# Kernel optimization log

Hardware: AMD Instinct MI355X
Metric: run time of the kernel (lower is better)

Reference implementation:

```python
import jax, jax.numpy as jnp
import numpy as np

B, S, D = 4, 2048, 1024


def setup_inputs() -> dict:
    key = jax.random.key(0)
    ks = jax.random.split(key, 9)
    scale = 1.0 / np.sqrt(D)
    x = jax.random.normal(ks[0], (B, S, D), dtype=jnp.float32)
    mask = jnp.tril(jnp.ones((S, S), dtype=jnp.int32))[None, :, :]  # causal, broadcast over batch
    Wq = jax.random.normal(ks[1], (D, D), dtype=jnp.float32) * scale
    bq = jax.random.normal(ks[2], (D,), dtype=jnp.float32) * 0.01
    Wk = jax.random.normal(ks[3], (D, D), dtype=jnp.float32) * scale
    bk = jax.random.normal(ks[4], (D,), dtype=jnp.float32) * 0.01
    Wv = jax.random.normal(ks[5], (D, D), dtype=jnp.float32) * scale
    bv = jax.random.normal(ks[6], (D,), dtype=jnp.float32) * 0.01
    Wo = jax.random.normal(ks[7], (D, D), dtype=jnp.float32) * scale
    bo = jax.random.normal(ks[8], (D,), dtype=jnp.float32) * 0.01
    return {"x": x, "mask": mask, "Wq": Wq, "bq": bq, "Wk": Wk, "bk": bk,
            "Wv": Wv, "bv": bv, "Wo": Wo, "bo": bo}


def reference(x, mask, Wq, bq, Wk, bk, Wv, bv, Wo, bo):
    # Linear projections (torch Linear: x @ W^T + b; here W stored as [in, out])
    Q = jnp.einsum('bsd,de->bse', x, Wq) + bq
    K = jnp.einsum('bsd,de->bse', x, Wk) + bk
    V = jnp.einsum('bsd,de->bse', x, Wv) + bv
    d_k = Q.shape[-1]
    scores = jnp.einsum('bqd,bkd->bqk', Q, K) / jnp.sqrt(jnp.float32(d_k))
    scores = jnp.where(mask == 0, jnp.float32(-jnp.inf), scores)
    attn_weights = jax.nn.softmax(scores, axis=-1)  # [B, S, S]
    attn_output = jnp.einsum('bqk,bkd->bqd', attn_weights, V)
    output = jnp.einsum('bsd,de->bse', attn_output, Wo) + bo
    return output, attn_weights
```

## Files before the change

kernel.cpp:

```cpp
#include <hip/hip_runtime.h>
#include <cstdint>
#include <cstddef>
#include <cmath>

typedef __bf16 bf16_t;
typedef bf16_t bf16x8 __attribute__((ext_vector_type(8)));
typedef bf16_t bf16x4 __attribute__((ext_vector_type(4)));
typedef float f32x4 __attribute__((ext_vector_type(4)));

constexpr int kB = 4;
constexpr int kS = 2048;
constexpr int kD = 1024;
constexpr int BM = 128, BN = 128, BK = 32;
constexpr int TILE_ELEMS = (BM + BN) * BK;

typedef __attribute__((address_space(1))) void as1void;
typedef __attribute__((address_space(3))) void as3void;

__device__ __forceinline__ void gload16(const void* g, void* l) {
  __builtin_amdgcn_global_load_lds((as1void*)g, (as3void*)l, 16, 0, 0);
}

__device__ __forceinline__ void wgbar() {
  asm volatile("" ::: "memory");
  __builtin_amdgcn_s_barrier();
  asm volatile("" ::: "memory");
}

__device__ __forceinline__ void gemm_mainloop(
    const bf16_t* __restrict__ A, int lda,
    const bf16_t* __restrict__ B, int ldb,
    int ksteps, bf16_t* lds, f32x4 acc[4][4]) {
  const int tid = threadIdx.x;
  const int w = tid >> 6, lane = tid & 63;
  const int srow = lane >> 2;
  const int scol = (lane & 3) << 3;
  const int wr = (w >> 1) << 6, wc = (w & 1) << 6;
  const int fr = lane & 15, kg = lane >> 4;

  const bf16_t* ga0 = A + (size_t)(w * 16 + srow) * lda + scol;
  const bf16_t* ga1 = A + (size_t)(64 + w * 16 + srow) * lda + scol;
  const bf16_t* gb0 = B + (size_t)(w * 16 + srow) * ldb + scol;
  const bf16_t* gb1 = B + (size_t)(64 + w * 16 + srow) * ldb + scol;
  const int oa0 = (w * 16) * BK;
  const int oa1 = (64 + w * 16) * BK;
  const int ob0 = BM * BK + (w * 16) * BK;
  const int ob1 = BM * BK + (64 + w * 16) * BK;

  gload16(ga0, lds + oa0);
  gload16(ga1, lds + oa1);
  gload16(gb0, lds + ob0);
  gload16(gb1, lds + ob1);
  ga0 += BK; ga1 += BK; gb0 += BK; gb1 += BK;
  __syncthreads();

  int cur = 0;
  for (int ks = 0; ks < ksteps; ++ks) {
    const int nxt = cur ^ 1;
    if (ks + 1 < ksteps) {
      bf16_t* nb = lds + nxt * TILE_ELEMS;
      gload16(ga0, nb + oa0);
      gload16(ga1, nb + oa1);
      gload16(gb0, nb + ob0);
      gload16(gb1, nb + ob1);
      ga0 += BK; ga1 += BK; gb0 += BK; gb1 += BK;
    }
    const bf16_t* cb = lds + cur * TILE_ELEMS;
    bf16x8 af[4], bfv[4];
#pragma unroll
    for (int m = 0; m < 4; ++m)
      af[m] = *(const bf16x8*)(cb + (wr + m * 16 + fr) * BK + kg * 8);
#pragma unroll
    for (int n = 0; n < 4; ++n)
      bfv[n] = *(const bf16x8*)(cb + BM * BK + (wc + n * 16 + fr) * BK + kg * 8);
#pragma unroll
    for (int m = 0; m < 4; ++m)
#pragma unroll
      for (int n = 0; n < 4; ++n)
        acc[m][n] = __builtin_amdgcn_mfma_f32_16x16x32_bf16(af[m], bfv[n],
                                                            acc[m][n], 0, 0, 0);
    __syncthreads();
    cur = nxt;
  }
}

__device__ __forceinline__ void gemm256_loop(
    const bf16_t* __restrict__ A, int lda,
    const bf16_t* __restrict__ B, int ldb,
    int nk, bf16_t* lds, f32x4 acc[8][4]) {
  const int tid = threadIdx.x;
  const int wid = tid >> 6, lane = tid & 63;
  const int wm = wid >> 2, wn = wid & 3;
  const int fr = lane & 15, kg = (lane >> 4) & 3;
  const int s_row = ((tid >> 7) << 4) | (tid & 15);
  const int s_col = ((tid >> 4) & 7) << 3;
  const bf16_t* pA = A + (size_t)s_row * lda + s_col;
  const bf16_t* pB = B + (size_t)s_row * ldb + s_col;
  const int ldst = wid << 9;

  auto stg = [&](int tt, int op, int h, int j) {
    const bf16_t* g = (op ? pB : pA) + (size_t)(h * 128 + j * 64) * (op ? ldb : lda)
                      + (size_t)tt * 64;
    bf16_t* d = lds + (((tt & 1) * 4 + op * 2 + h) * 8192) + j * 4096 + ldst;
    gload16(g, d);
  };

#pragma unroll
  for (int h = 0; h < 2; ++h)
#pragma unroll
    for (int j = 0; j < 2; ++j) { stg(0, 0, h, j); stg(0, 1, h, j); }
  stg(1, 1, 0, 0); stg(1, 1, 0, 1); stg(1, 1, 1, 0); stg(1, 1, 1, 1);
  stg(1, 0, 0, 0); stg(1, 0, 1, 0);
  asm volatile("s_waitcnt vmcnt(6)" ::: "memory");
  wgbar();

  const int arow = kg * 128 + fr * 8;
  for (int t = 0; t < nk; ++t) {
    const bf16_t* sb = lds + (t & 1) * 32768;
    const bf16_t* aslot = sb + wm * 8192;
    const bf16_t* bslot = sb + (2 + (wn >> 1)) * 8192 + (wn & 1) * 4096;
    bf16x8 bF[4][2];
#pragma unroll
    for (int q = 0; q < 4; ++q) {
      bf16x8 aF[2][2];
#pragma unroll
      for (int mi = 0; mi < 2; ++mi)
#pragma unroll
        for (int ks = 0; ks < 2; ++ks)
          aF[mi][ks] = *(const bf16x8*)(aslot + (2 * q + mi) * 1024 + ks * 512 + arow);
      if (q == 0) {
#pragma unroll
        for (int n = 0; n < 4; ++n)
#pragma unroll
          for (int ks = 0; ks < 2; ++ks)
            bF[n][ks] = *(const bf16x8*)(bslot + n * 1024 + ks * 512 + arow);
      }
      if (q == 0)      { if (t + 1 <= nk - 1) { stg(t + 1, 0, 0, 1); stg(t + 1, 0, 1, 1); } }
      else if (q == 1) { if (t + 2 <= nk - 1) { stg(t + 2, 1, 0, 0); stg(t + 2, 1, 0, 1); } }
      else if (q == 2) { if (t + 2 <= nk - 1) { stg(t + 2, 1, 1, 0); stg(t + 2, 1, 1, 1); } }
      else             { if (t + 2 <= nk - 1) { stg(t + 2, 0, 0, 0); stg(t + 2, 0, 1, 0); } }
      wgbar();
      __builtin_amdgcn_s_setprio(1);
#pragma unroll
      for (int mi = 0; mi < 2; ++mi)
#pragma unroll
        for (int n = 0; n < 4; ++n)
#pragma unroll
          for (int ks = 0; ks < 2; ++ks)
            acc[2 * q + mi][n] = __builtin_amdgcn_mfma_f32_16x16x32_bf16(
                aF[mi][ks], bF[n][ks], acc[2 * q + mi][n], 0, 0, 0);
      __builtin_amdgcn_s_setprio(0);
      asm volatile("s_waitcnt lgkmcnt(0)" ::: "memory");
      if (q == 3 && t < nk - 1) {
        if (t + 2 <= nk - 1) asm volatile("s_waitcnt vmcnt(6)" ::: "memory");
        else                 asm volatile("s_waitcnt vmcnt(0)" ::: "memory");
      }
      wgbar();
    }
  }
}


__global__ __launch_bounds__(512, 2)
void k_qk256(const bf16_t* __restrict__ A, const bf16_t* __restrict__ WT,
             const float* __restrict__ bq, const float* __restrict__ bk,
             bf16_t* __restrict__ Qb, bf16_t* __restrict__ Kb) {
  __shared__ bf16_t lds[65536];
  const int id = blockIdx.x;
  const int swz = (id & 7) * 32 + (id >> 3);
  const int mb = swz >> 3, nb = swz & 7;
  const int m0 = mb * 256, n0 = nb * 256;
  f32x4 acc[8][4] = {};
  gemm256_loop(A + (size_t)m0 * kD, kD, WT + (size_t)n0 * kD, kD,
               kD / 64, lds, acc);
  const int lane = threadIdx.x & 63, wid = threadIdx.x >> 6;
  const int wm = wid >> 2, wn = wid & 3, fr = lane & 15, kgr = lane >> 4;
  const int which = n0 >> 10;
  bf16_t* C = which == 0 ? Qb : Kb;
  const float* bias = which == 0 ? bq : bk;
#pragma unroll
  for (int n = 0; n < 4; ++n) {
    const int col = (n0 & 1023) + wn * 64 + n * 16 + fr;
    const float bvv = bias[col];
#pragma unroll
    for (int m = 0; m < 8; ++m)
#pragma unroll
      for (int i = 0; i < 4; ++i) {
        const int row = m0 + wm * 128 + m * 16 + kgr * 4 + i;
        C[(size_t)row * kD + col] = (bf16_t)(acc[m][n][i] + bvv);
      }
  }
}

__global__ __launch_bounds__(256)
void k_scores_v(const bf16_t* __restrict__ Q, const bf16_t* __restrict__ K,
                float* __restrict__ Sc,
                const bf16_t* __restrict__ X, const bf16_t* __restrict__ WvT,
                const float* __restrict__ bv, bf16_t* __restrict__ VT) {
  __shared__ bf16_t lds[2 * TILE_ELEMS];
  const int id = blockIdx.x;
  const int wid0 = (id & 7) * 192 + (id >> 3);
  const int tid = threadIdx.x, w = tid >> 6, lane = tid & 63;
  const int wr = (w >> 1) << 6, wc = (w & 1) << 6, fr = lane & 15, kg = lane >> 4;
  if (wid0 < 544) {
    const int b = wid0 / 136, t = wid0 % 136;
    int by = (int)((sqrtf(8.f * t + 1.f) - 1.f) * 0.5f);
    while ((by + 1) * (by + 2) / 2 <= t) ++by;
    while (by * (by + 1) / 2 > t) --by;
    const int bx = t - by * (by + 1) / 2;
    const int m0 = by * BM, n0 = bx * BN;
    f32x4 acc[4][4] = {};
    gemm_mainloop(Q + (size_t)b * kS * kD + (size_t)m0 * kD, kD,
                  K + (size_t)b * kS * kD + (size_t)n0 * kD, kD, kD / BK, lds, acc);
    float* Sb = Sc + (size_t)b * kS * kS;
#pragma unroll
    for (int m = 0; m < 4; ++m)
#pragma unroll
      for (int n = 0; n < 4; ++n)
#pragma unroll
        for (int i = 0; i < 4; ++i) {
          const int row = m0 + wr + m * 16 + kg * 4 + i;
          const int col = n0 + wc + n * 16 + fr;
          Sb[(size_t)row * kS + col] = acc[m][n][i] * 0.03125f;
        }
  } else if (wid0 < 1024) {
    const int zid = wid0 - 544;
    const int b = zid / 120, u = zid % 120;
    int r = (int)((1.f + sqrtf(8.f * u + 1.f)) * 0.5f);
    while (r * (r - 1) / 2 > u) --r;
    while ((r + 1) * r / 2 <= u) ++r;
    const int c = u - r * (r - 1) / 2;
    const int by = c, bx = r;
    float* base = Sc + (size_t)b * kS * kS + (size_t)by * BM * kS + bx * BN;
    const f32x4 z = {0.f, 0.f, 0.f, 0.f};
    for (int i = tid; i < 128 * 32; i += 256) {
      const int row = i >> 5, c4 = i & 31;
      ((f32x4*)(base + (size_t)row * kS))[c4] = z;
    }
  } else {
    const int vid = wid0 - 1024;
    const int m0 = (vid >> 3) * BM, n0 = (vid & 7) * BN;
    f32x4 acc[4][4] = {};
    gemm_mainloop(X + (size_t)m0 * kD, kD, WvT + (size_t)n0 * kD, kD,
                  kD / BK, lds, acc);
#pragma unroll
    for (int n = 0; n < 4; ++n) {
      const int col = n0 + wc + n * 16 + fr;
      const float bvv = bv[col];
#pragma unroll
      for (int m = 0; m < 4; ++m)
#pragma unroll
        for (int i = 0; i < 4; ++i) {
          const int row = m0 + wr + m * 16 + kg * 4 + i;
          const int b = row >> 11, s = row & (kS - 1);
          VT[((size_t)b * kD + col) * kS + s] = (bf16_t)(acc[m][n][i] + bvv);
        }
    }
  }
}

__global__ __launch_bounds__(256)
void k_softmax(float* __restrict__ P, bf16_t* __restrict__ Pb) {
  const int row = blockIdx.x;
  const int q = row & (kS - 1);
  const int L = q + 1;
  const int nch = (q >> 2) + 1;
  const int nB = ((q & ~127) + 128) >> 2;
  float* p = P + (size_t)row * kS;
  f32x4* p4 = (f32x4*)p;
  bf16x4* pb4 = (bf16x4*)(Pb + (size_t)row * kS);
  const int tid = threadIdx.x;
  const int c0 = tid, c1 = 256 + tid;
  f32x4 v0 = {-1e30f, -1e30f, -1e30f, -1e30f}, v1 = v0;
  if (c0 < nch) v0 = p4[c0];
  if (c1 < nch) v1 = p4[c1];
#pragma unroll
  for (int j = 0; j < 4; ++j) {
    if (4 * c0 + j >= L) v0[j] = -1e30f;
    if (4 * c1 + j >= L) v1[j] = -1e30f;
  }
  float mx = -1e30f;
#pragma unroll
  for (int j = 0; j < 4; ++j) mx = fmaxf(mx, fmaxf(v0[j], v1[j]));
#pragma unroll
  for (int s2 = 32; s2 >= 1; s2 >>= 1) mx = fmaxf(mx, __shfl_xor(mx, s2));
  __shared__ float red[8];
  if ((tid & 63) == 0) red[tid >> 6] = mx;
  __syncthreads();
  mx = fmaxf(fmaxf(red[0], red[1]), fmaxf(red[2], red[3]));
  f32x4 e0, e1;
  float sm = 0.f;
#pragma unroll
  for (int j = 0; j < 4; ++j) {
    e0[j] = (4 * c0 + j < L) ? __expf(v0[j] - mx) : 0.f;
    e1[j] = (4 * c1 + j < L) ? __expf(v1[j] - mx) : 0.f;
    sm += e0[j] + e1[j];
  }
#pragma unroll
  for (int s2 = 32; s2 >= 1; s2 >>= 1) sm += __shfl_xor(sm, s2);
  if ((tid & 63) == 0) red[4 + (tid >> 6)] = sm;
  __syncthreads();
  const float inv = 1.f / (red[4] + red[5] + red[6] + red[7]);
  if (c0 < nB) {
    f32x4 o; bf16x4 ob;
#pragma unroll
    for (int j = 0; j < 4; ++j) { o[j] = e0[j] * inv; ob[j] = (bf16_t)o[j]; }
    p4[c0] = o; pb4[c0] = ob;
  }
  if (c1 < nB) {
    f32x4 o; bf16x4 ob;
#pragma unroll
    for (int j = 0; j < 4; ++j) { o[j] = e1[j] * inv; ob[j] = (bf16_t)o[j]; }
    p4[c1] = o; pb4[c1] = ob;
  }
}

__global__ __launch_bounds__(256)
void k_gemm_pv(const bf16_t* __restrict__ P, const bf16_t* __restrict__ VT,
               bf16_t* __restrict__ AO) {
  const int bx = blockIdx.x, b = blockIdx.z;
  const int by = (int)gridDim.y - 1 - (int)blockIdx.y;
  __shared__ bf16_t lds[2 * TILE_ELEMS];
  const int m0 = by * BM, n0 = bx * BN;
  const int ksteps = (m0 + BM) / BK;
  f32x4 acc[4][4] = {};
  gemm_mainloop(P + (size_t)b * kS * kS + (size_t)m0 * kS, kS,
                VT + (size_t)b * kD * kS + (size_t)n0 * kS, kS, ksteps, lds, acc);
  bf16_t* AOb = AO + (size_t)b * kS * kD;
  const int tid = threadIdx.x, w = tid >> 6, lane = tid & 63;
  const int wr = (w >> 1) << 6, wc = (w & 1) << 6, fr = lane & 15, kg = lane >> 4;
#pragma unroll
  for (int m = 0; m < 4; ++m)
#pragma unroll
    for (int n = 0; n < 4; ++n)
#pragma unroll
      for (int i = 0; i < 4; ++i) {
        const int row = m0 + wr + m * 16 + kg * 4 + i;
        const int col = n0 + wc + n * 16 + fr;
        AOb[(size_t)row * kD + col] = (bf16_t)acc[m][n][i];
      }
}

__global__ __launch_bounds__(256)
void k_gemm_out(const bf16_t* __restrict__ A, const bf16_t* __restrict__ Bw,
                const float* __restrict__ bias, float* __restrict__ C) {
  __shared__ bf16_t lds[2 * TILE_ELEMS];
  const int id = blockIdx.x;
  const int swz = (id & 7) * 64 + (id >> 3);
  const int m0 = (swz >> 3) * BM, n0 = (swz & 7) * BN;
  f32x4 acc[4][4] = {};
  gemm_mainloop(A + (size_t)m0 * kD, kD, Bw + (size_t)n0 * kD, kD, kD / BK, lds, acc);
  const int tid = threadIdx.x, w = tid >> 6, lane = tid & 63;
  const int wr = (w >> 1) << 6, wc = (w & 1) << 6, fr = lane & 15, kg = lane >> 4;
#pragma unroll
  for (int n = 0; n < 4; ++n) {
    const int col = n0 + wc + n * 16 + fr;
    const float bv = bias[col];
#pragma unroll
    for (int m = 0; m < 4; ++m)
#pragma unroll
      for (int i = 0; i < 4; ++i) {
        const int row = m0 + wr + m * 16 + kg * 4 + i;
        C[(size_t)row * kD + col] = acc[m][n][i] + bv;
      }
  }
}

__global__ __launch_bounds__(256)
void k_prep(const float* __restrict__ X, bf16_t* __restrict__ Y,
            const float* __restrict__ W0, const float* __restrict__ W1,
            const float* __restrict__ W2, const float* __restrict__ W3,
            bf16_t* __restrict__ T0, bf16_t* __restrict__ T1,
            bf16_t* __restrict__ T2, bf16_t* __restrict__ T3) {
  const int tx = threadIdx.x & 31, ty = threadIdx.x >> 5;
  if (blockIdx.z == 4) {
    const size_t n4 = (size_t)kB * kS * kD / 4;
    size_t i = ((size_t)blockIdx.y * 32 + blockIdx.x) * 256 + threadIdx.x;
    const size_t stride = (size_t)1024 * 256;
    const float4* X4 = (const float4*)X;
    bf16x4* Y4 = (bf16x4*)Y;
    for (; i < n4; i += stride) {
      const float4 v = X4[i];
      bf16x4 o = {(bf16_t)v.x, (bf16_t)v.y, (bf16_t)v.z, (bf16_t)v.w};
      Y4[i] = o;
    }
    return;
  }
  const float* W = blockIdx.z == 0 ? W0 : blockIdx.z == 1 ? W1 : blockIdx.z == 2 ? W2 : W3;
  bf16_t* T = blockIdx.z == 0 ? T0 : blockIdx.z == 1 ? T1 : blockIdx.z == 2 ? T2 : T3;
  __shared__ float t[32][33];
  const int x0 = blockIdx.x * 32, y0 = blockIdx.y * 32;
#pragma unroll
  for (int j = 0; j < 4; ++j)
    t[ty + 8 * j][tx] = W[(size_t)(y0 + ty + 8 * j) * kD + x0 + tx];
  __syncthreads();
#pragma unroll
  for (int j = 0; j < 4; ++j)
    T[(size_t)(x0 + ty + 8 * j) * kD + y0 + tx] = (bf16_t)t[tx][ty + 8 * j];
}

extern "C" void kernel_launch(void* const* d_in, const int* in_sizes, int n_in,
                              void* d_out, int out_size, void* d_ws, size_t ws_size,
                              hipStream_t stream) {
  (void)in_sizes; (void)n_in; (void)out_size; (void)ws_size;
  const float* x  = (const float*)d_in[0];
  const float* Wq = (const float*)d_in[2];
  const float* bq = (const float*)d_in[3];
  const float* Wk = (const float*)d_in[4];
  const float* bk = (const float*)d_in[5];
  const float* Wv = (const float*)d_in[6];
  const float* bv = (const float*)d_in[7];
  const float* Wo = (const float*)d_in[8];
  const float* bo = (const float*)d_in[9];

  float* out  = (float*)d_out;
  float* Pout = out + (size_t)kB * kS * kD;

  bf16_t* WqT = (bf16_t*)d_ws;
  bf16_t* WkT = WqT + (size_t)kD * kD;
  bf16_t* WvT = WkT + (size_t)kD * kD;
  bf16_t* WoT = WvT + (size_t)kD * kD;
  bf16_t* Qb  = WoT + (size_t)kD * kD;
  bf16_t* Kb  = Qb + (size_t)kB * kS * kD;
  bf16_t* VTb = Kb + (size_t)kB * kS * kD;
  bf16_t* Pb  = VTb + (size_t)kB * kS * kD;
  bf16_t* AOb = Pb + (size_t)kB * kS * kS;
  bf16_t* xb  = AOb + (size_t)kB * kS * kD;

  k_prep<<<dim3(32, 32, 5), 256, 0, stream>>>(x, xb, Wq, Wk, Wv, Wo,
                                              WqT, WkT, WvT, WoT);
  k_qk256<<<256, 512, 0, stream>>>(xb, WqT, bq, bk, Qb, Kb);
  k_scores_v<<<1536, 256, 0, stream>>>(Qb, Kb, Pout, xb, WvT, bv, VTb);
  k_softmax<<<kB * kS, 256, 0, stream>>>(Pout, Pb);
  k_gemm_pv<<<dim3(8, 16, kB), 256, 0, stream>>>(Pb, VTb, AOb);
  k_gemm_out<<<512, 256, 0, stream>>>(AOb, WoT, bo, out);
}
```

Measured before the change: 214.5 us.

## Use atomic work-queue persistent scheduling in scores/V kernel, GEMMs before zero tiles

Replaces the static block-to-work mapping in the fused scores/V-projection kernel with a persistent grid of 1024 blocks that pull work items from a global atomic counter. Work is reordered so all GEMM tiles (QK^T and V projection) are dispatched first and the cheap zero-fill tiles of the upper triangle last, to balance load and reduce tail imbalance. The counter is reset in the prep kernel. It adds per-item atomic and barrier overhead and depends on the counter reset ordering across kernels.

```diff
diff --git a/kernel.cpp b/kernel.cpp
--- a/kernel.cpp
+++ b/kernel.cpp
@@ -196,65 +196,71 @@
 void k_scores_v(const bf16_t* __restrict__ Q, const bf16_t* __restrict__ K,
                 float* __restrict__ Sc,
                 const bf16_t* __restrict__ X, const bf16_t* __restrict__ WvT,
-                const float* __restrict__ bv, bf16_t* __restrict__ VT) {
+                const float* __restrict__ bv, bf16_t* __restrict__ VT,
+                unsigned int* __restrict__ ctr) {
   __shared__ bf16_t lds[2 * TILE_ELEMS];
-  const int id = blockIdx.x;
-  const int wid0 = (id & 7) * 192 + (id >> 3);
+  __shared__ unsigned int sid;
   const int tid = threadIdx.x, w = tid >> 6, lane = tid & 63;
   const int wr = (w >> 1) << 6, wc = (w & 1) << 6, fr = lane & 15, kg = lane >> 4;
-  if (wid0 < 544) {
-    const int b = wid0 / 136, t = wid0 % 136;
-    int by = (int)((sqrtf(8.f * t + 1.f) - 1.f) * 0.5f);
-    while ((by + 1) * (by + 2) / 2 <= t) ++by;
-    while (by * (by + 1) / 2 > t) --by;
-    const int bx = t - by * (by + 1) / 2;
-    const int m0 = by * BM, n0 = bx * BN;
-    f32x4 acc[4][4] = {};
-    gemm_mainloop(Q + (size_t)b * kS * kD + (size_t)m0 * kD, kD,
-                  K + (size_t)b * kS * kD + (size_t)n0 * kD, kD, kD / BK, lds, acc);
-    float* Sb = Sc + (size_t)b * kS * kS;
-#pragma unroll
-    for (int m = 0; m < 4; ++m)
-#pragma unroll
-      for (int n = 0; n < 4; ++n)
-#pragma unroll
-        for (int i = 0; i < 4; ++i) {
-          const int row = m0 + wr + m * 16 + kg * 4 + i;
-          const int col = n0 + wc + n * 16 + fr;
-          Sb[(size_t)row * kS + col] = acc[m][n][i] * 0.03125f;
-        }
-  } else if (wid0 < 1024) {
-    const int zid = wid0 - 544;
-    const int b = zid / 120, u = zid % 120;
-    int r = (int)((1.f + sqrtf(8.f * u + 1.f)) * 0.5f);
-    while (r * (r - 1) / 2 > u) --r;
-    while ((r + 1) * r / 2 <= u) ++r;
-    const int c = u - r * (r - 1) / 2;
-    const int by = c, bx = r;
-    float* base = Sc + (size_t)b * kS * kS + (size_t)by * BM * kS + bx * BN;
-    const f32x4 z = {0.f, 0.f, 0.f, 0.f};
-    for (int i = tid; i < 128 * 32; i += 256) {
-      const int row = i >> 5, c4 = i & 31;
-      ((f32x4*)(base + (size_t)row * kS))[c4] = z;
-    }
-  } else {
-    const int vid = wid0 - 1024;
-    const int m0 = (vid >> 3) * BM, n0 = (vid & 7) * BN;
-    f32x4 acc[4][4] = {};
-    gemm_mainloop(X + (size_t)m0 * kD, kD, WvT + (size_t)n0 * kD, kD,
-                  kD / BK, lds, acc);
-#pragma unroll
-    for (int n = 0; n < 4; ++n) {
-      const int col = n0 + wc + n * 16 + fr;
-      const float bvv = bv[col];
+  for (;;) {
+    __syncthreads();
+    if (tid == 0) sid = atomicAdd(ctr, 1u);
+    __syncthreads();
+    const unsigned int id = sid;
+    if (id >= 1536u) return;
+    if (id < 544u) {
+      const int b = id / 136, t = id % 136;
+      int by = (int)((sqrtf(8.f * t + 1.f) - 1.f) * 0.5f);
+      while ((by + 1) * (by + 2) / 2 <= t) ++by;
+      while (by * (by + 1) / 2 > t) --by;
+      const int bx = t - by * (by + 1) / 2;
+      const int m0 = by * BM, n0 = bx * BN;
+      f32x4 acc[4][4] = {};
+      gemm_mainloop(Q + (size_t)b * kS * kD + (size_t)m0 * kD, kD,
+                    K + (size_t)b * kS * kD + (size_t)n0 * kD, kD, kD / BK, lds, acc);
+      float* Sb = Sc + (size_t)b * kS * kS;
 #pragma unroll
       for (int m = 0; m < 4; ++m)
 #pragma unroll
-        for (int i = 0; i < 4; ++i) {
-          const int row = m0 + wr + m * 16 + kg * 4 + i;
-          const int b = row >> 11, s = row & (kS - 1);
-          VT[((size_t)b * kD + col) * kS + s] = (bf16_t)(acc[m][n][i] + bvv);
-        }
+        for (int n = 0; n < 4; ++n)
+#pragma unroll
+          for (int i = 0; i < 4; ++i) {
+            const int row = m0 + wr + m * 16 + kg * 4 + i;
+            const int col = n0 + wc + n * 16 + fr;
+            Sb[(size_t)row * kS + col] = acc[m][n][i] * 0.03125f;
+          }
+    } else if (id < 1056u) {
+      const int vid = id - 544;
+      const int m0 = (vid >> 3) * BM, n0 = (vid & 7) * BN;
+      f32x4 acc[4][4] = {};
+      gemm_mainloop(X + (size_t)m0 * kD, kD, WvT + (size_t)n0 * kD, kD,
+                    kD / BK, lds, acc);
+#pragma unroll
+      for (int n = 0; n < 4; ++n) {
+        const int col = n0 + wc + n * 16 + fr;
+        const float bvv = bv[col];
+#pragma unroll
+        for (int m = 0; m < 4; ++m)
+#pragma unroll
+          for (int i = 0; i < 4; ++i) {
+            const int row = m0 + wr + m * 16 + kg * 4 + i;
+            const int b = row >> 11, s = row & (kS - 1);
+            VT[((size_t)b * kD + col) * kS + s] = (bf16_t)(acc[m][n][i] + bvv);
+          }
+      }
+    } else {
+      const int zid = id - 1056;
+      const int b = zid / 120, u = zid % 120;
+      int r = (int)((1.f + sqrtf(8.f * u + 1.f)) * 0.5f);
+      while (r * (r - 1) / 2 > u) --r;
+      while ((r + 1) * r / 2 <= u) ++r;
+      const int c = u - r * (r - 1) / 2;
+      float* base = Sc + (size_t)b * kS * kS + (size_t)c * BM * kS + r * BN;
+      const f32x4 z = {0.f, 0.f, 0.f, 0.f};
+      for (int i = tid; i < 128 * 32; i += 256) {
+        const int row = i >> 5, c4 = i & 31;
+        ((f32x4*)(base + (size_t)row * kS))[c4] = z;
+      }
     }
   }
 }
@@ -371,9 +377,11 @@
             const float* __restrict__ W0, const float* __restrict__ W1,
             const float* __restrict__ W2, const float* __restrict__ W3,
             bf16_t* __restrict__ T0, bf16_t* __restrict__ T1,
-            bf16_t* __restrict__ T2, bf16_t* __restrict__ T3) {
+            bf16_t* __restrict__ T2, bf16_t* __restrict__ T3,
+            unsigned int* __restrict__ ctr) {
   const int tx = threadIdx.x & 31, ty = threadIdx.x >> 5;
   if (blockIdx.z == 4) {
+    if (blockIdx.x == 0 && blockIdx.y == 0 && threadIdx.x == 0) ctr[0] = 0u;
     const size_t n4 = (size_t)kB * kS * kD / 4;
     size_t i = ((size_t)blockIdx.y * 32 + blockIdx.x) * 256 + threadIdx.x;
     const size_t stride = (size_t)1024 * 256;
@@ -426,11 +434,12 @@
   bf16_t* Pb  = VTb + (size_t)kB * kS * kD;
   bf16_t* AOb = Pb + (size_t)kB * kS * kS;
   bf16_t* xb  = AOb + (size_t)kB * kS * kD;
+  unsigned int* ctr = (unsigned int*)(xb + (size_t)kB * kS * kD);
 
   k_prep<<<dim3(32, 32, 5), 256, 0, stream>>>(x, xb, Wq, Wk, Wv, Wo,
-                                              WqT, WkT, WvT, WoT);
+                                              WqT, WkT, WvT, WoT, ctr);
   k_qk256<<<256, 512, 0, stream>>>(xb, WqT, bq, bk, Qb, Kb);
-  k_scores_v<<<1536, 256, 0, stream>>>(Qb, Kb, Pout, xb, WvT, bv, VTb);
+  k_scores_v<<<1024, 256, 0, stream>>>(Qb, Kb, Pout, xb, WvT, bv, VTb, ctr);
   k_softmax<<<kB * kS, 256, 0, stream>>>(Pout, Pb);
   k_gemm_pv<<<dim3(8, 16, kB), 256, 0, stream>>>(Pb, VTb, AOb);
   k_gemm_out<<<512, 256, 0, stream>>>(AOb, WoT, bo, out);
```

Measured after the change: 222.3 us. +3.6%, slower.
